# Optimization experiments

Hardware: AMD Instinct MI355X
Metric: run time of the kernel (lower is better)

Reference implementation:

```python
import jax, jax.numpy as jnp
import numpy as np
import math

B, S, HID, NH = 4, 256, 512, 8
D = HID // NH


def setup_inputs() -> dict:
    key = jax.random.key(0)
    ks = jax.random.split(key, 12)
    inp = {
        "q_hidden_states": jax.random.normal(ks[0], (B, S, HID), dtype=jnp.float32),
        "k_hidden_states": jax.random.normal(ks[1], (B, S, HID), dtype=jnp.float32),
        "v_hidden_states": jax.random.normal(ks[2], (B, S, HID), dtype=jnp.float32),
        "Wq": jax.random.normal(ks[3], (HID, HID), dtype=jnp.float32) * 0.02,
        "bq": jnp.zeros((HID,), dtype=jnp.float32),
        "Wk": jax.random.normal(ks[4], (HID, HID), dtype=jnp.float32) * 0.02,
        "bk": jnp.zeros((HID,), dtype=jnp.float32),
        "Wv": jax.random.normal(ks[5], (HID, HID), dtype=jnp.float32) * 0.02,
        "bv": jnp.zeros((HID,), dtype=jnp.float32),
        "rel_table": (jax.random.normal(ks[6], (8, HID), dtype=jnp.float32) * 0.02).at[0].set(0.0),  # padding_idx=0
        "edge_type": jax.random.randint(ks[7], (B, S, S), 0, 8, dtype=jnp.int32),
        "trans_mask": jax.random.randint(ks[8], (B, S, S), 0, 2, dtype=jnp.int32),
    }
    return inp


def _split_heads(x):
    # [B, S, HID] -> [B, NH, S, D]
    b, s, _ = x.shape
    return x.reshape(b, s, NH, D).transpose(0, 2, 1, 3)


def reference(q_hidden_states, k_hidden_states, v_hidden_states,
              Wq, bq, Wk, bk, Wv, bv, rel_table, edge_type, trans_mask):
    scale = 1.0 / math.sqrt(D)
    Q0 = _split_heads(q_hidden_states @ Wq + bq)  # [B,H,S,D]
    K0 = _split_heads(k_hidden_states @ Wk + bk)
    V0 = _split_heads(v_hidden_states @ Wv + bv)

    # Faithful vectorization of the torch loop:
    # at iteration i, Q and K have accumulated sum_{t<=i} rel_layer_t, and only
    # row i of the full QK^T is kept. Hence:
    #   scores[b,h,i,j] = (Q0[i] + C[i,i]) . (K0[j] + C[i,j]) / sqrt(D)
    # where C[t,p] = cumsum over t of rel_emb[:, t, p].
    R = rel_table[edge_type]                                  # [B,S,S,HID]
    C = jnp.cumsum(R.reshape(B, S, S, NH, D), axis=1)         # [B,t,p,H,D]
    idx = jnp.arange(S)
    diagC = C[:, idx, idx].transpose(0, 2, 1, 3)              # [B,H,S,D]: C[:,i,i]
    qrow = Q0 + diagC                                         # [B,H,S,D]

    scores = (jnp.einsum('bhid,bhjd->bhij', qrow, K0)
              + jnp.einsum('bhid,bijhd->bhij', qrow, C)) * scale

    scores = jnp.where(trans_mask[:, None, :, :] == 0, -1e9, scores)
    probs = jax.nn.softmax(scores, axis=-1)  # dropout omitted (eval mode)

    ctx = jnp.einsum('bhij,bhjd->bhid', probs, V0)            # [B,H,S,D]
    return ctx.transpose(0, 2, 1, 3).reshape(B, S, HID)
```

## Files before the change

### kernel.cpp

```cpp
#include <hip/hip_runtime.h>
#include <math.h>

#define BB 4
#define SS 256
#define HID 512
#define NHD 8
#define DD 64
#define IT 16

typedef __attribute__((ext_vector_type(8))) short short8v;
typedef __attribute__((ext_vector_type(4))) float f32x4;

static __device__ __forceinline__ ushort f2bf(float x) {
    uint u = __float_as_uint(x);
    uint r = u + 0x7fffu + ((u >> 16) & 1u);
    return (ushort)(r >> 16);
}
static __device__ __forceinline__ float bf2f(ushort h) {
    return __uint_as_float(((uint)h) << 16);
}
static __device__ __forceinline__ void cvt8(const float4& a, const float4& b,
                                            short8v& hi, short8v& lo) {
    ushort h;
    h = f2bf(a.x); hi[0] = (short)h; lo[0] = (short)f2bf(a.x - bf2f(h));
    h = f2bf(a.y); hi[1] = (short)h; lo[1] = (short)f2bf(a.y - bf2f(h));
    h = f2bf(a.z); hi[2] = (short)h; lo[2] = (short)f2bf(a.z - bf2f(h));
    h = f2bf(a.w); hi[3] = (short)h; lo[3] = (short)f2bf(a.w - bf2f(h));
    h = f2bf(b.x); hi[4] = (short)h; lo[4] = (short)f2bf(b.x - bf2f(h));
    h = f2bf(b.y); hi[5] = (short)h; lo[5] = (short)f2bf(b.y - bf2f(h));
    h = f2bf(b.z); hi[6] = (short)h; lo[6] = (short)f2bf(b.z - bf2f(h));
    h = f2bf(b.w); hi[7] = (short)h; lo[7] = (short)f2bf(b.w - bf2f(h));
}

__global__ __launch_bounds__(256) void gemm_cnt(
    const float* __restrict__ xq, const float* __restrict__ xk, const float* __restrict__ xv,
    const float* __restrict__ wq, const float* __restrict__ wk, const float* __restrict__ wv,
    const float* __restrict__ bq, const float* __restrict__ bk, const float* __restrict__ bv,
    float* __restrict__ oq, float* __restrict__ ok, float* __restrict__ ov,
    const int* __restrict__ edge, uint4* __restrict__ cnt)
{
    const int bid = blockIdx.x;
    const int t = threadIdx.x;
    const int wave = t >> 6, lane = t & 63;

    if (bid >= 384) {
        const int col = (bid - 384) * 4 + wave;
        const int b = col / SS, j = col % SS;
        uint4 run = make_uint4(0, 0, 0, 0);
        uint4 c[4];
        #pragma unroll
        for (int r = 0; r < 4; ++r) {
            const int e = edge[((size_t)(b * SS + lane * 4 + r)) * SS + j];
            const unsigned inc = 1u << ((e & 1) * 16);
            const int comp = e >> 1;
            run.x += (comp == 0) ? inc : 0u;
            run.y += (comp == 1) ? inc : 0u;
            run.z += (comp == 2) ? inc : 0u;
            run.w += (comp == 3) ? inc : 0u;
            c[r] = run;
        }
        uint4 tot = run;
        #pragma unroll
        for (int off = 1; off < 64; off <<= 1) {
            uint4 s;
            s.x = __shfl_up((int)tot.x, off);
            s.y = __shfl_up((int)tot.y, off);
            s.z = __shfl_up((int)tot.z, off);
            s.w = __shfl_up((int)tot.w, off);
            if (lane >= off) { tot.x += s.x; tot.y += s.y; tot.z += s.z; tot.w += s.w; }
        }
        const uint4 excl = make_uint4(tot.x - run.x, tot.y - run.y, tot.z - run.z, tot.w - run.w);
        #pragma unroll
        for (int r = 0; r < 4; ++r) {
            uint4 o = make_uint4(excl.x + c[r].x, excl.y + c[r].y, excl.z + c[r].z, excl.w + c[r].w);
            cnt[((size_t)(b * SS + lane * 4 + r)) * SS + j] = o;
        }
        return;
    }

    __shared__ ushort As_hi[64][40];
    __shared__ ushort As_lo[64][40];
    __shared__ ushort Bs_hi[64][40];
    __shared__ ushort Bs_lo[64][40];

    const int z = bid / 128, rr = bid % 128;
    const float* X    = (z == 0) ? xq : (z == 1) ? xk : xv;
    const float* W    = (z == 0) ? wq : (z == 1) ? wk : wv;
    const float* bias = (z == 0) ? bq : (z == 1) ? bk : bv;
    float*       out  = (z == 0) ? oq : (z == 1) ? ok : ov;
    const int bm = (rr & 15) * 64, bn = (rr >> 4) * 64;

    const int wr = wave >> 1, wc = wave & 1;
    const int sm = t >> 2, sk = (t & 3) * 8;
    const int wn = t & 63, wks = (t >> 6) * 8;
    const int fr = lane & 15, kb = (lane >> 4) * 8;

    f32x4 acc[2][2] = {};

    for (int k0 = 0; k0 < HID; k0 += 32) {
        {
            const float* xp = &X[(size_t)(bm + sm) * HID + k0 + sk];
            const float4 a0 = *(const float4*)&xp[0];
            const float4 a1 = *(const float4*)&xp[4];
            short8v h8, l8;
            cvt8(a0, a1, h8, l8);
            *(short8v*)&As_hi[sm][sk] = h8;
            *(short8v*)&As_lo[sm][sk] = l8;
        }
        {
            float wv8[8];
            #pragma unroll
            for (int j = 0; j < 8; ++j)
                wv8[j] = W[(size_t)(k0 + wks + j) * HID + bn + wn];
            short8v wh, wl;
            #pragma unroll
            for (int j = 0; j < 8; ++j) {
                const ushort h = f2bf(wv8[j]);
                wh[j] = (short)h;
                wl[j] = (short)f2bf(wv8[j] - bf2f(h));
            }
            *(short8v*)&Bs_hi[wn][wks] = wh;
            *(short8v*)&Bs_lo[wn][wks] = wl;
        }
        __syncthreads();

        short8v ah[2], al[2], bh[2], bl[2];
        #pragma unroll
        for (int mi = 0; mi < 2; ++mi) {
            ah[mi] = *(const short8v*)&As_hi[wr * 32 + mi * 16 + fr][kb];
            al[mi] = *(const short8v*)&As_lo[wr * 32 + mi * 16 + fr][kb];
        }
        #pragma unroll
        for (int ni = 0; ni < 2; ++ni) {
            bh[ni] = *(const short8v*)&Bs_hi[wc * 32 + ni * 16 + fr][kb];
            bl[ni] = *(const short8v*)&Bs_lo[wc * 32 + ni * 16 + fr][kb];
        }
        #pragma unroll
        for (int mi = 0; mi < 2; ++mi)
            #pragma unroll
            for (int ni = 0; ni < 2; ++ni) {
                acc[mi][ni] = __builtin_amdgcn_mfma_f32_16x16x32_bf16(ah[mi], bh[ni], acc[mi][ni], 0, 0, 0);
                acc[mi][ni] = __builtin_amdgcn_mfma_f32_16x16x32_bf16(ah[mi], bl[ni], acc[mi][ni], 0, 0, 0);
                acc[mi][ni] = __builtin_amdgcn_mfma_f32_16x16x32_bf16(al[mi], bh[ni], acc[mi][ni], 0, 0, 0);
            }
        __syncthreads();
    }

    const int r0 = bm + wr * 32 + (lane >> 4) * 4;
    const int c0 = bn + wc * 32 + (lane & 15);
    #pragma unroll
    for (int ni = 0; ni < 2; ++ni) {
        const float bia = bias[c0 + ni * 16];
        #pragma unroll
        for (int mi = 0; mi < 2; ++mi)
            #pragma unroll
            for (int q = 0; q < 4; ++q)
                out[(size_t)(r0 + mi * 16 + q) * HID + c0 + ni * 16] = acc[mi][ni][q] + bia;
    }
}

__global__ __launch_bounds__(256) void attn_fused(
    const float* __restrict__ Q0,
    const float* __restrict__ K0,
    const float* __restrict__ V0,
    const float* __restrict__ rel,
    const uint4* __restrict__ cnt,
    const int* __restrict__ mask,
    float* __restrict__ out)
{
    const int x = blockIdx.x;
    const int it = x & 15;
    const int h  = (x >> 4) & 7;
    const int b  = x >> 7;
    const int i0 = it * IT;
    const int t = threadIdx.x, wave = t >> 6, lane = t & 63;

    __shared__ ushort qhi[16][72];
    __shared__ ushort qlo[16][72];
    __shared__ float qre_s[IT][8];
    __shared__ float s_t[SS][20];
    __shared__ float vtile[64][68];

    const int pi = t >> 4, pd = t & 15;
    float4 qr4;
    {
        const float4 q4 = *(const float4*)&Q0[((size_t)(b * SS + i0 + pi)) * HID + h * DD + pd * 4];
        const uint4 cv = cnt[((size_t)(b * SS + i0 + pi)) * SS + (i0 + pi)];
        float c[8];
        c[0] = (float)(cv.x & 0xffff); c[1] = (float)(cv.x >> 16);
        c[2] = (float)(cv.y & 0xffff); c[3] = (float)(cv.y >> 16);
        c[4] = (float)(cv.z & 0xffff); c[5] = (float)(cv.z >> 16);
        c[6] = (float)(cv.w & 0xffff); c[7] = (float)(cv.w >> 16);
        float o0 = q4.x, o1 = q4.y, o2 = q4.z, o3 = q4.w;
        #pragma unroll
        for (int e = 0; e < 8; ++e) {
            const float4 r4 = *(const float4*)&rel[e * HID + h * DD + pd * 4];
            o0 += c[e] * r4.x; o1 += c[e] * r4.y; o2 += c[e] * r4.z; o3 += c[e] * r4.w;
        }
        qr4.x = o0; qr4.y = o1; qr4.z = o2; qr4.w = o3;
        ushort4 h4, l4;
        h4.x = f2bf(o0); l4.x = f2bf(o0 - bf2f(h4.x));
        h4.y = f2bf(o1); l4.y = f2bf(o1 - bf2f(h4.y));
        h4.z = f2bf(o2); l4.z = f2bf(o2 - bf2f(h4.z));
        h4.w = f2bf(o3); l4.w = f2bf(o3 - bf2f(h4.w));
        *(ushort4*)&qhi[pi][pd * 4] = h4;
        *(ushort4*)&qlo[pi][pd * 4] = l4;
    }
    {
        float r[8];
        #pragma unroll
        for (int e = 0; e < 8; ++e) {
            const float4 rr = *(const float4*)&rel[e * HID + h * DD + pd * 4];
            r[e] = qr4.x * rr.x + qr4.y * rr.y + qr4.z * rr.z + qr4.w * rr.w;
        }
        #pragma unroll
        for (int e = 0; e < 8; ++e) {
            float v = r[e];
            v += __shfl_xor(v, 1);
            v += __shfl_xor(v, 2);
            v += __shfl_xor(v, 4);
            v += __shfl_xor(v, 8);
            r[e] = v;
        }
        float sel = 0.f;
        #pragma unroll
        for (int e = 0; e < 8; ++e) if (pd == e) sel = r[e];
        if (pd < 8) qre_s[pi][pd] = sel;
    }
    __syncthreads();

    {
        const int fr = lane & 15, kb8 = (lane >> 4) * 8;
        const int jt = wave;
        const int ib = (lane >> 4) * 4;

        short8v qh[2], ql[2];
        #pragma unroll
        for (int ks = 0; ks < 2; ++ks) {
            qh[ks] = *(const short8v*)&qhi[fr][ks * 32 + kb8];
            ql[ks] = *(const short8v*)&qlo[fr][ks * 32 + kb8];
        }
        float4 qa[4], qb[4];
        #pragma unroll
        for (int q = 0; q < 4; ++q) {
            qa[q] = *(const float4*)&qre_s[ib + q][0];
            qb[q] = *(const float4*)&qre_s[ib + q][4];
        }

        #pragma unroll
        for (int jf = 0; jf < 4; ++jf) {
            const int j = jt * 64 + jf * 16 + fr;
            const float* Kr = &K0[((size_t)(b * SS + j)) * HID + h * DD];
            f32x4 acc = {};
            #pragma unroll
            for (int ks = 0; ks < 2; ++ks) {
                const float4 k0v = *(const float4*)&Kr[ks * 32 + kb8];
                const float4 k1v = *(const float4*)&Kr[ks * 32 + kb8 + 4];
                short8v kh, kl;
                cvt8(k0v, k1v, kh, kl);
                acc = __builtin_amdgcn_mfma_f32_16x16x32_bf16(qh[ks], kh, acc, 0, 0, 0);
                acc = __builtin_amdgcn_mfma_f32_16x16x32_bf16(qh[ks], kl, acc, 0, 0, 0);
                acc = __builtin_amdgcn_mfma_f32_16x16x32_bf16(ql[ks], kh, acc, 0, 0, 0);
            }
            float sv[4];
            #pragma unroll
            for (int q = 0; q < 4; ++q) {
                const int i = ib + q;
                const uint4 cv = cnt[((size_t)(b * SS + i0 + i)) * SS + j];
                float s = acc[q]
                    + qa[q].x * (float)(cv.x & 0xffff) + qa[q].y * (float)(cv.x >> 16)
                    + qa[q].z * (float)(cv.y & 0xffff) + qa[q].w * (float)(cv.y >> 16)
                    + qb[q].x * (float)(cv.z & 0xffff) + qb[q].y * (float)(cv.z >> 16)
                    + qb[q].z * (float)(cv.w & 0xffff) + qb[q].w * (float)(cv.w >> 16);
                s *= 0.125f;
                const int m = mask[((size_t)(b * SS + i0 + i)) * SS + j];
                sv[q] = m ? s : -1e9f;
            }
            float4 w4; w4.x = sv[0]; w4.y = sv[1]; w4.z = sv[2]; w4.w = sv[3];
            *(float4*)&s_t[j][ib] = w4;
        }
    }
    __syncthreads();

    {
        #pragma unroll
        for (int rr = 0; rr < 4; ++rr) {
            const int i = wave * 4 + rr;
            float v0 = s_t[lane][i], v1 = s_t[lane + 64][i],
                  v2 = s_t[lane + 128][i], v3 = s_t[lane + 192][i];
            float mx = fmaxf(fmaxf(v0, v1), fmaxf(v2, v3));
            #pragma unroll
            for (int off = 32; off > 0; off >>= 1) mx = fmaxf(mx, __shfl_xor(mx, off));
            float e0 = __expf(v0 - mx), e1 = __expf(v1 - mx),
                  e2 = __expf(v2 - mx), e3 = __expf(v3 - mx);
            float sm = e0 + e1 + e2 + e3;
            #pragma unroll
            for (int off = 32; off > 0; off >>= 1) sm += __shfl_xor(sm, off);
            const float inv = 1.f / sm;
            s_t[lane][i] = e0 * inv;
            s_t[lane + 64][i] = e1 * inv;
            s_t[lane + 128][i] = e2 * inv;
            s_t[lane + 192][i] = e3 * inv;
        }
    }
    __syncthreads();

    {
        const int iq = wave;
        const int jsub = (t >> 4) & 3, dq = t & 15;
        float o[4][4] = {};
        for (int jt = 0; jt < 4; ++jt) {
            {
                const int jr = t >> 2, seg = t & 3;
                const float* src = &V0[((size_t)(b * SS + jt * 64 + jr)) * HID + h * DD + seg * 16];
                #pragma unroll
                for (int qq = 0; qq < 4; ++qq)
                    *(float4*)&vtile[jr][seg * 16 + qq * 4] = *(const float4*)&src[qq * 4];
            }
            __syncthreads();
            #pragma unroll
            for (int jj = 0; jj < 16; ++jj) {
                const int j = jsub * 16 + jj;
                const float4 p4 = *(const float4*)&s_t[jt * 64 + j][iq * 4];
                const float4 v4 = *(const float4*)&vtile[j][dq * 4];
                o[0][0] += p4.x * v4.x; o[0][1] += p4.x * v4.y;
                o[0][2] += p4.x * v4.z; o[0][3] += p4.x * v4.w;
                o[1][0] += p4.y * v4.x; o[1][1] += p4.y * v4.y;
                o[1][2] += p4.y * v4.z; o[1][3] += p4.y * v4.w;
                o[2][0] += p4.z * v4.x; o[2][1] += p4.z * v4.y;
                o[2][2] += p4.z * v4.z; o[2][3] += p4.z * v4.w;
                o[3][0] += p4.w * v4.x; o[3][1] += p4.w * v4.y;
                o[3][2] += p4.w * v4.z; o[3][3] += p4.w * v4.w;
            }
            __syncthreads();
        }
        #pragma unroll
        for (int r = 0; r < 4; ++r)
            #pragma unroll
            for (int c = 0; c < 4; ++c) {
                float v = o[r][c];
                v += __shfl_xor(v, 16);
                v += __shfl_xor(v, 32);
                o[r][c] = v;
            }
        float sel0 = 0.f, sel1 = 0.f, sel2 = 0.f, sel3 = 0.f;
        #pragma unroll
        for (int r = 0; r < 4; ++r)
            if (r == jsub) { sel0 = o[r][0]; sel1 = o[r][1]; sel2 = o[r][2]; sel3 = o[r][3]; }
        const int i = iq * 4 + jsub;
        float4 ov; ov.x = sel0; ov.y = sel1; ov.z = sel2; ov.w = sel3;
        *(float4*)&out[((size_t)(b * SS + i0 + i)) * HID + h * DD + dq * 4] = ov;
    }
}

extern "C" void kernel_launch(void* const* d_in, const int* in_sizes, int n_in,
                              void* d_out, int out_size, void* d_ws, size_t ws_size,
                              hipStream_t stream) {
    const float* q_hs = (const float*)d_in[0];
    const float* k_hs = (const float*)d_in[1];
    const float* v_hs = (const float*)d_in[2];
    const float* Wq   = (const float*)d_in[3];
    const float* bq   = (const float*)d_in[4];
    const float* Wk   = (const float*)d_in[5];
    const float* bk   = (const float*)d_in[6];
    const float* Wv   = (const float*)d_in[7];
    const float* bv   = (const float*)d_in[8];
    const float* rel  = (const float*)d_in[9];
    const int* edge   = (const int*)d_in[10];
    const int* mask   = (const int*)d_in[11];
    float* out = (float*)d_out;

    char* ws = (char*)d_ws;
    float*  Q    = (float*)(ws);
    float*  K0   = (float*)(ws + (2u  << 20));
    float*  V0   = (float*)(ws + (4u  << 20));
    uint4*  cnt  = (uint4*)(ws + (6u  << 20));

    gemm_cnt<<<dim3(640), 256, 0, stream>>>(q_hs, k_hs, v_hs, Wq, Wk, Wv,
                                            bq, bk, bv, Q, K0, V0, edge, cnt);
    attn_fused<<<dim3(BB * NHD * (SS / IT)), 256, 0, stream>>>(Q, K0, V0, rel, cnt, mask, out);
}
```

Before: 113.1 us.

## Pre-split K/V to bf16 hi/lo in GEMM epilogue and use MFMA for PV

The projection GEMM epilogue now writes K as bf16 hi/lo pairs and V transposed per head as bf16 hi/lo pairs. The attention kernel then loads K fragments directly instead of converting them from fp32 in every block. The softmax probabilities are stored as bf16 hi/lo in shared memory, and the P·V product uses split-bf16 MFMA reading transposed V straight from global memory, replacing the scalar FMA loop and the V tile staging. This removes redundant conversion work and the scalar PV compute. The trade-offs are the split-precision approximation on P and V, and uncoalesced scattered ushort4 stores for the V transpose.

```diff
diff --git a/kernel.cpp b/kernel.cpp
--- a/kernel.cpp
+++ b/kernel.cpp
@@ -36,7 +36,8 @@
     const float* __restrict__ xq, const float* __restrict__ xk, const float* __restrict__ xv,
     const float* __restrict__ wq, const float* __restrict__ wk, const float* __restrict__ wv,
     const float* __restrict__ bq, const float* __restrict__ bk, const float* __restrict__ bv,
-    float* __restrict__ oq, float* __restrict__ ok, float* __restrict__ ov,
+    float* __restrict__ Qo, ushort* __restrict__ Khi, ushort* __restrict__ Klo,
+    ushort* __restrict__ Vthi, ushort* __restrict__ Vtlo,
     const int* __restrict__ edge, uint4* __restrict__ cnt)
 {
     const int bid = blockIdx.x;
@@ -87,7 +88,6 @@
     const float* X    = (z == 0) ? xq : (z == 1) ? xk : xv;
     const float* W    = (z == 0) ? wq : (z == 1) ? wk : wv;
     const float* bias = (z == 0) ? bq : (z == 1) ? bk : bv;
-    float*       out  = (z == 0) ? oq : (z == 1) ? ok : ov;
     const int bm = (rr & 15) * 64, bn = (rr >> 4) * 64;
 
     const int wr = wave >> 1, wc = wave & 1;
@@ -148,21 +148,59 @@
 
     const int r0 = bm + wr * 32 + (lane >> 4) * 4;
     const int c0 = bn + wc * 32 + (lane & 15);
-    #pragma unroll
-    for (int ni = 0; ni < 2; ++ni) {
-        const float bia = bias[c0 + ni * 16];
-        #pragma unroll
-        for (int mi = 0; mi < 2; ++mi)
-            #pragma unroll
-            for (int q = 0; q < 4; ++q)
-                out[(size_t)(r0 + mi * 16 + q) * HID + c0 + ni * 16] = acc[mi][ni][q] + bia;
+    if (z == 0) {
+        #pragma unroll
+        for (int ni = 0; ni < 2; ++ni) {
+            const float bia = bias[c0 + ni * 16];
+            #pragma unroll
+            for (int mi = 0; mi < 2; ++mi)
+                #pragma unroll
+                for (int q = 0; q < 4; ++q)
+                    Qo[(size_t)(r0 + mi * 16 + q) * HID + c0 + ni * 16] = acc[mi][ni][q] + bia;
+        }
+    } else if (z == 1) {
+        #pragma unroll
+        for (int ni = 0; ni < 2; ++ni) {
+            const float bia = bias[c0 + ni * 16];
+            #pragma unroll
+            for (int mi = 0; mi < 2; ++mi)
+                #pragma unroll
+                for (int q = 0; q < 4; ++q) {
+                    const float v = acc[mi][ni][q] + bia;
+                    const ushort h = f2bf(v);
+                    const size_t o = (size_t)(r0 + mi * 16 + q) * HID + c0 + ni * 16;
+                    Khi[o] = h;
+                    Klo[o] = f2bf(v - bf2f(h));
+                }
+        }
+    } else {
+        #pragma unroll
+        for (int ni = 0; ni < 2; ++ni) {
+            const int c = c0 + ni * 16;
+            const float bia = bias[c];
+            const int hh = c >> 6, dd = c & 63;
+            #pragma unroll
+            for (int mi = 0; mi < 2; ++mi) {
+                const int tok = r0 + mi * 16;
+                const int b2 = tok / SS, s0 = tok % SS;
+                ushort4 h4, l4;
+                float v;
+                v = acc[mi][ni][0] + bia; h4.x = f2bf(v); l4.x = f2bf(v - bf2f(h4.x));
+                v = acc[mi][ni][1] + bia; h4.y = f2bf(v); l4.y = f2bf(v - bf2f(h4.y));
+                v = acc[mi][ni][2] + bia; h4.z = f2bf(v); l4.z = f2bf(v - bf2f(h4.z));
+                v = acc[mi][ni][3] + bia; h4.w = f2bf(v); l4.w = f2bf(v - bf2f(h4.w));
+                const size_t o = (((size_t)b2 * NHD + hh) * DD + dd) * SS + s0;
+                *(ushort4*)&Vthi[o] = h4;
+                *(ushort4*)&Vtlo[o] = l4;
+            }
+        }
     }
 }
 
 __global__ __launch_bounds__(256) void attn_fused(
     const float* __restrict__ Q0,
-    const float* __restrict__ K0,
-    const float* __restrict__ V0,
+    const ushort* __restrict__ Khi, const ushort* __restrict__ Klo,
+    const ushort* __restrict__ Vthi, const ushort* __restrict__ Vtlo,
     const float* __restrict__ rel,
     const uint4* __restrict__ cnt,
     const int* __restrict__ mask,
@@ -179,7 +217,8 @@
     __shared__ ushort qlo[16][72];
     __shared__ float qre_s[IT][8];
     __shared__ float s_t[SS][20];
-    __shared__ float vtile[64][68];
+    __shared__ ushort pb_hi[16][264];
+    __shared__ ushort pb_lo[16][264];
 
     const int pi = t >> 4, pd = t & 15;
     float4 qr4;
@@ -229,8 +268,9 @@
     }
     __syncthreads();
 
+    const int fr = lane & 15, kb8 = (lane >> 4) * 8;
+
     {
-        const int fr = lane & 15, kb8 = (lane >> 4) * 8;
         const int jt = wave;
         const int ib = (lane >> 4) * 4;
 
@@ -250,14 +290,12 @@
         #pragma unroll
         for (int jf = 0; jf < 4; ++jf) {
             const int j = jt * 64 + jf * 16 + fr;
-            const float* Kr = &K0[((size_t)(b * SS + j)) * HID + h * DD];
+            const size_t kbase = ((size_t)(b * SS + j)) * HID + h * DD;
             f32x4 acc = {};
             #pragma unroll
             for (int ks = 0; ks < 2; ++ks) {
-                const float4 k0v = *(const float4*)&Kr[ks * 32 + kb8];
-                const float4 k1v = *(const float4*)&Kr[ks * 32 + kb8 + 4];
-                short8v kh, kl;
-                cvt8(k0v, k1v, kh, kl);
+                const short8v kh = *(const short8v*)&Khi[kbase + ks * 32 + kb8];
+                const short8v kl = *(const short8v*)&Klo[kbase + ks * 32 + kb8];
                 acc = __builtin_amdgcn_mfma_f32_16x16x32_bf16(qh[ks], kh, acc, 0, 0, 0);
                 acc = __builtin_amdgcn_mfma_f32_16x16x32_bf16(qh[ks], kl, acc, 0, 0, 0);
                 acc = __builtin_amdgcn_mfma_f32_16x16x32_bf16(ql[ks], kh, acc, 0, 0, 0);
@@ -297,59 +335,38 @@
             #pragma unroll
             for (int off = 32; off > 0; off >>= 1) sm += __shfl_xor(sm, off);
             const float inv = 1.f / sm;
-            s_t[lane][i] = e0 * inv;
-            s_t[lane + 64][i] = e1 * inv;
-            s_t[lane + 128][i] = e2 * inv;
-            s_t[lane + 192][i] = e3 * inv;
+            e0 *= inv; e1 *= inv; e2 *= inv; e3 *= inv;
+            ushort h;
+            h = f2bf(e0); pb_hi[i][lane      ] = h; pb_lo[i][lane      ] = f2bf(e0 - bf2f(h));
+            h = f2bf(e1); pb_hi[i][lane +  64] = h; pb_lo[i][lane +  64] = f2bf(e1 - bf2f(h));
+            h = f2bf(e2); pb_hi[i][lane + 128] = h; pb_lo[i][lane + 128] = f2bf(e2 - bf2f(h));
+            h = f2bf(e3); pb_hi[i][lane + 192] = h; pb_lo[i][lane + 192] = f2bf(e3 - bf2f(h));
         }
     }
     __syncthreads();
 
     {
-        const int iq = wave;
-        const int jsub = (t >> 4) & 3, dq = t & 15;
-        float o[4][4] = {};
-        for (int jt = 0; jt < 4; ++jt) {
-            {
-                const int jr = t >> 2, seg = t & 3;
-                const float* src = &V0[((size_t)(b * SS + jt * 64 + jr)) * HID + h * DD + seg * 16];
-                #pragma unroll
-                for (int qq = 0; qq < 4; ++qq)
-                    *(float4*)&vtile[jr][seg * 16 + qq * 4] = *(const float4*)&src[qq * 4];
-            }
-            __syncthreads();
-            #pragma unroll
-            for (int jj = 0; jj < 16; ++jj) {
-                const int j = jsub * 16 + jj;
-                const float4 p4 = *(const float4*)&s_t[jt * 64 + j][iq * 4];
-                const float4 v4 = *(const float4*)&vtile[j][dq * 4];
-                o[0][0] += p4.x * v4.x; o[0][1] += p4.x * v4.y;
-                o[0][2] += p4.x * v4.z; o[0][3] += p4.x * v4.w;
-                o[1][0] += p4.y * v4.x; o[1][1] += p4.y * v4.y;
-                o[1][2] += p4.y * v4.z; o[1][3] += p4.y * v4.w;
-                o[2][0] += p4.z * v4.x; o[2][1] += p4.z * v4.y;
-                o[2][2] += p4.z * v4.z; o[2][3] += p4.z * v4.w;
-                o[3][0] += p4.w * v4.x; o[3][1] += p4.w * v4.y;
-                o[3][2] += p4.w * v4.z; o[3][3] += p4.w * v4.w;
-            }
-            __syncthreads();
-        }
-        #pragma unroll
-        for (int r = 0; r < 4; ++r)
-            #pragma unroll
-            for (int c = 0; c < 4; ++c) {
-                float v = o[r][c];
-                v += __shfl_xor(v, 16);
-                v += __shfl_xor(v, 32);
-                o[r][c] = v;
-            }
-        float sel0 = 0.f, sel1 = 0.f, sel2 = 0.f, sel3 = 0.f;
-        #pragma unroll
-        for (int r = 0; r < 4; ++r)
-            if (r == jsub) { sel0 = o[r][0]; sel1 = o[r][1]; sel2 = o[r][2]; sel3 = o[r][3]; }
-        const int i = iq * 4 + jsub;
-        float4 ov; ov.x = sel0; ov.y = sel1; ov.z = sel2; ov.w = sel3;
-        *(float4*)&out[((size_t)(b * SS + i0 + i)) * HID + h * DD + dq * 4] = ov;
+        const int dcol = wave * 16 + fr;
+        const size_t vbase = (((size_t)b * NHD + h) * DD + dcol) * SS;
+        f32x4 opv = {};
+        #pragma unroll
+        for (int jt = 0; jt < 4; ++jt)
+            #pragma unroll
+            for (int c2 = 0; c2 < 2; ++c2) {
+                const int joff = jt * 64 + c2 * 32 + kb8;
+                const short8v ph = *(const short8v*)&pb_hi[fr][joff];
+                const short8v pl = *(const short8v*)&pb_lo[fr][joff];
+                const short8v vh = *(const short8v*)&Vthi[vbase + joff];
+                const short8v vl = *(const short8v*)&Vtlo[vbase + joff];
+                opv = __builtin_amdgcn_mfma_f32_16x16x32_bf16(ph, vh, opv, 0, 0, 0);
+                opv = __builtin_amdgcn_mfma_f32_16x16x32_bf16(pl, vh, opv, 0, 0, 0);
+                opv = __builtin_amdgcn_mfma_f32_16x16x32_bf16(ph, vl, opv, 0, 0, 0);
+            }
+        #pragma unroll
+        for (int q = 0; q < 4; ++q) {
+            const int i = (lane >> 4) * 4 + q;
+            out[((size_t)(b * SS + i0 + i)) * HID + h * DD + dcol] = opv[q];
+        }
     }
 }
 
@@ -372,11 +389,15 @@
 
     char* ws = (char*)d_ws;
     float*  Q    = (float*)(ws);
-    float*  K0   = (float*)(ws + (2u  << 20));
-    float*  V0   = (float*)(ws + (4u  << 20));
-    uint4*  cnt  = (uint4*)(ws + (6u  << 20));
+    ushort* Khi  = (ushort*)(ws + (2u << 20));
+    ushort* Klo  = (ushort*)(ws + (3u << 20));
+    ushort* Vthi = (ushort*)(ws + (4u << 20));
+    ushort* Vtlo = (ushort*)(ws + (5u << 20));
+    uint4*  cnt  = (uint4*)(ws + (6u << 20));
 
     gemm_cnt<<<dim3(640), 256, 0, stream>>>(q_hs, k_hs, v_hs, Wq, Wk, Wv,
-                                            bq, bk, bv, Q, K0, V0, edge, cnt);
-    attn_fused<<<dim3(BB * NHD * (SS / IT)), 256, 0, stream>>>(Q, K0, V0, rel, cnt, mask, out);
-}
+                                            bq, bk, bv, Q, Khi, Klo, Vthi, Vtlo,
+                                            edge, cnt);
+    attn_fused<<<dim3(BB * NHD * (SS / IT)), 256, 0, stream>>>(Q, Khi, Klo, Vthi, Vtlo,
+                                                               rel, cnt, mask, out);
+}
```

Result: faster. 110.5 us (-2.3%).
